# Kernel optimization log

Measured on AMD Instinct MI355X. Metric: run time of the kernel, lower is better.

The kernel has to match this reference:

```python
import jax, jax.numpy as jnp
import numpy as np

N_NODES = 50000
N_EDGES = 600000
IN_CH = 300
HID = 128
N_CLASSES = 2
N_GRAPHS = 128
BN_EPS = 1e-5


def setup_inputs() -> dict:
    key = jax.random.key(0)
    ks = jax.random.split(key, 24)
    x = jax.random.normal(ks[0], (N_NODES, IN_CH), dtype=jnp.float32)
    edge_index = jax.random.randint(ks[1], (2, N_EDGES), 0, N_NODES, dtype=jnp.int64)
    batch = jnp.sort(jax.random.randint(ks[2], (N_NODES,), 0, N_GRAPHS, dtype=jnp.int64))

    def glorot(k, shape):
        fan_in, fan_out = shape
        s = jnp.sqrt(2.0 / (fan_in + fan_out)).astype(jnp.float32)
        return jax.random.normal(k, shape, dtype=jnp.float32) * s

    inp = {"x": x, "edge_index": edge_index, "batch": batch}
    # SAGEConv params: W_l (neighbor branch), W_r (root branch), bias
    dims = [(IN_CH, HID), (HID, HID), (HID, HID)]
    for i, (din, dout) in enumerate(dims, start=1):
        inp[f"W{i}l"] = glorot(ks[3 * i], (din, dout))
        inp[f"W{i}r"] = glorot(ks[3 * i + 1], (din, dout))
        inp[f"b{i}"] = jnp.zeros((dout,), dtype=jnp.float32)
        inp[f"g{i}"] = jnp.ones((dout,), dtype=jnp.float32)   # BN gamma
        inp[f"be{i}"] = jnp.zeros((dout,), dtype=jnp.float32)  # BN beta
    inp["Wc"] = glorot(ks[20], (HID, N_CLASSES))
    inp["bc"] = jnp.zeros((N_CLASSES,), dtype=jnp.float32)
    return inp


def _sage_conv(x, src, dst, Wl, Wr, b):
    # mean-aggregate neighbor features (messages flow src -> dst)
    msg_sum = jax.ops.segment_sum(x[src], dst, num_segments=N_NODES)
    deg = jax.ops.segment_sum(jnp.ones((src.shape[0],), dtype=x.dtype), dst,
                              num_segments=N_NODES)
    mean = msg_sum / jnp.maximum(deg, 1.0)[:, None]
    return mean @ Wl + x @ Wr + b


def _bn_relu(h, gamma, beta):
    mu = jnp.mean(h, axis=0)
    var = jnp.var(h, axis=0)
    h = (h - mu) * jax.lax.rsqrt(var + BN_EPS) * gamma + beta
    return jax.nn.relu(h)


def reference(x, edge_index, batch,
              W1l, W1r, b1, g1, be1,
              W2l, W2r, b2, g2, be2,
              W3l, W3r, b3, g3, be3,
              Wc, bc):
    src, dst = edge_index[0], edge_index[1]
    h = _bn_relu(_sage_conv(x, src, dst, W1l, W1r, b1), g1, be1)
    h = _bn_relu(_sage_conv(h, src, dst, W2l, W2r, b2), g2, be2)
    h = _bn_relu(_sage_conv(h, src, dst, W3l, W3r, b3), g3, be3)
    # global mean pool per graph
    pooled = jax.ops.segment_sum(h, batch, num_segments=N_GRAPHS)
    cnt = jax.ops.segment_sum(jnp.ones((h.shape[0],), dtype=h.dtype), batch,
                              num_segments=N_GRAPHS)
    hg = pooled / jnp.maximum(cnt, 1.0)[:, None]
    out = hg @ Wc + bc
    return out, hg
```

## Files before the change

kernel.cpp:

```cpp
#include <hip/hip_runtime.h>

#define N_NODES   50000
#define N_EDGES   600000
#define IN_CH     300
#define HID       128
#define N_CLASSES 2
#define N_GRAPHS  128
#define BN_EPS    1e-5f

#define NB ((N_NODES + 511) / 512)
#define KP1 320
#define NREP 32
#define DEGB ((N_EDGES + 255) / 256)

typedef __attribute__((ext_vector_type(8))) short bf8_t;
typedef __attribute__((ext_vector_type(4))) float f4_t;

__device__ __forceinline__ unsigned short f2bf(float x) {
    union { float f; unsigned u; } q; q.f = x;
    unsigned r = q.u + 0x7fffu + ((q.u >> 16) & 1u);
    return (unsigned short)(r >> 16);
}
__device__ __forceinline__ float bf2f(unsigned short h) {
    union { float f; unsigned u; } q; q.u = ((unsigned)h) << 16; return q.f;
}

__device__ __forceinline__ void async_cp16(const void* g, void* l) {
    __builtin_amdgcn_global_load_lds(
        (const __attribute__((address_space(1))) unsigned int*)g,
        (__attribute__((address_space(3))) unsigned int*)l, 16, 0, 0);
}

__global__ __launch_bounds__(256) void deg_prepw(const int* __restrict__ dst,
                                                 int* __restrict__ ideg,
                                                 const float* __restrict__ W1l,
                                                 const float* __restrict__ W1r,
                                                 const float* __restrict__ W2l,
                                                 const float* __restrict__ W2r,
                                                 const float* __restrict__ W3l,
                                                 const float* __restrict__ W3r,
                                                 unsigned short* __restrict__ B1h,
                                                 unsigned short* __restrict__ B1l,
                                                 unsigned short* __restrict__ B2h,
                                                 unsigned short* __restrict__ B2l,
                                                 unsigned short* __restrict__ B3h,
                                                 unsigned short* __restrict__ B3l) {
    int b = blockIdx.x;
    if (b < DEGB) {
        int e = b * 256 + threadIdx.x;
        if (e < N_EDGES) atomicAdd(&ideg[dst[e]], 1);
        return;
    }
    int pb = b - DEGB;
    int layer, base;
    if (pb < 320)      { layer = 0; base = pb; }
    else if (pb < 448) { layer = 1; base = pb - 320; }
    else               { layer = 2; base = pb - 448; }
    int Kp = (layer == 0) ? KP1 : HID;
    int K  = (layer == 0) ? IN_CH : HID;
    const float* Wl = (layer == 0) ? W1l : ((layer == 1) ? W2l : W3l);
    const float* Wr = (layer == 0) ? W1r : ((layer == 1) ? W2r : W3r);
    unsigned short* Bh = (layer == 0) ? B1h : ((layer == 1) ? B2h : B3h);
    unsigned short* Bl = (layer == 0) ? B1l : ((layer == 1) ? B2l : B3l);
    int idx = base * 256 + threadIdx.x;
    int n = idx / Kp;
    int k = idx - n * Kp;
    float v = 0.f;
    if (k < K) v = (n < 128) ? Wl[k * 128 + n] : Wr[k * 128 + (n - 128)];
    unsigned short h = f2bf(v);
    unsigned short l = f2bf(v - bf2f(h));
    Bh[idx] = h;
    Bl[idx] = l;
}

__global__ __launch_bounds__(256) void scan_fused(const int* __restrict__ ideg,
                                                  int* __restrict__ row_start,
                                                  float* __restrict__ invdeg,
                                                  int* __restrict__ bsum,
                                                  int* __restrict__ bflag) {
    int b = blockIdx.x, t = threadIdx.x;
    int lane = t & 63, wv = t >> 6;
    int i0 = b * 512 + t * 2;
    int v0 = 0, v1 = 0;
    if (i0 < N_NODES) {
        int2 v = *(const int2*)&ideg[i0];
        v0 = v.x; v1 = v.y;
    }
    int tot = v0 + v1;
    int s = tot;
#pragma unroll
    for (int d = 1; d < 64; d <<= 1) {
        int u = __shfl_up(s, d);
        if (lane >= d) s += u;
    }
    __shared__ int ws[4];
    if (lane == 63) ws[wv] = s;
    __syncthreads();
    int btot = ws[0] + ws[1] + ws[2] + ws[3];
    if (t == 0) {
        atomicExch(&bsum[b], btot);
        __threadfence();
        atomicExch(&bflag[b], 1);
    }
    int part = 0;
    if (t < b) {
        while (atomicAdd(&bflag[t], 0) == 0) {}
        part = atomicAdd(&bsum[t], 0);
    }
#pragma unroll
    for (int d = 1; d < 64; d <<= 1) part += __shfl_down(part, d);
    __shared__ int ps[4];
    if (lane == 0) ps[wv] = part;
    __syncthreads();
    int boff = ps[0] + ps[1] + ps[2] + ps[3];
    int woff = 0;
    for (int w = 0; w < wv; ++w) woff += ws[w];
    int base = boff + woff + (s - tot);
    if (i0 < N_NODES) {
        row_start[i0]     = base;
        row_start[i0 + 1] = base + v0;
        invdeg[i0]     = 1.0f / fmaxf((float)v0, 1.0f);
        invdeg[i0 + 1] = 1.0f / fmaxf((float)v1, 1.0f);
    }
    if (t == 0 && b == NB - 1) row_start[N_NODES] = boff + btot;
}

__global__ __launch_bounds__(256) void fill_kernel(const int* __restrict__ src,
                                                   const int* __restrict__ dst,
                                                   const int* __restrict__ row_start,
                                                   int* __restrict__ cursor,
                                                   int* __restrict__ csr_src) {
    int e = blockIdx.x * 256 + threadIdx.x;
    if (e >= N_EDGES) return;
    int d = dst[e];
    int pos = row_start[d] + atomicAdd(&cursor[d], 1);
    csr_src[pos] = src[e];
}

__global__ __launch_bounds__(256) void gemm_mfma_x(const float* __restrict__ X,
                                                   int M,
                                                   const unsigned short* __restrict__ Bhi,
                                                   const unsigned short* __restrict__ Blo,
                                                   const float* __restrict__ bias,
                                                   unsigned short* __restrict__ C0,
                                                   float* __restrict__ C1) {
    __shared__ __align__(16) unsigned short sAh[64 * 32];
    __shared__ __align__(16) unsigned short sAl[64 * 32];
    __shared__ __align__(16) unsigned short sBh[256 * 32];
    __shared__ __align__(16) unsigned short sBl[256 * 32];

    const int tid  = threadIdx.x;
    const int lane = tid & 63;
    const int wave = tid >> 6;
    const int l16  = lane & 15;
    const int quad = lane >> 4;
    const long m0  = (long)blockIdx.x * 64;
    const int  n0  = wave * 64;

    f4_t acc[4][4];
#pragma unroll
    for (int mt = 0; mt < 4; ++mt)
#pragma unroll
        for (int nt = 0; nt < 4; ++nt) acc[mt][nt] = (f4_t){0.f, 0.f, 0.f, 0.f};

    const int ar  = tid >> 2;
    const int cl  = tid & 3;
    const int cpa = cl ^ ((ar >> 1) & 3);
    long agr = m0 + ar;
    if (agr >= M) agr = M - 1;
    const float* gX = X + agr * IN_CH;

    const int cg = ((lane & 3) ^ ((lane >> 3) & 3)) * 8;
    const unsigned short* gBh[4];
    const unsigned short* gBl[4];
    unsigned short* lBh[4];
    unsigned short* lBl[4];
#pragma unroll
    for (int j = 0; j < 4; ++j) {
        long br = wave * 64 + j * 16 + (lane >> 2);
        gBh[j] = Bhi + br * KP1 + cg;
        gBl[j] = Blo + br * KP1 + cg;
        lBh[j] = &sBh[wave * 2048 + j * 512];
        lBl[j] = &sBl[wave * 2048 + j * 512];
    }
    const int rsw = (quad ^ ((l16 >> 1) & 3)) * 8;

    for (int k0 = 0; k0 < KP1; k0 += 32) {
#pragma unroll
        for (int j = 0; j < 4; ++j) {
            async_cp16(gBh[j] + k0, lBh[j]);
            async_cp16(gBl[j] + k0, lBl[j]);
        }
        float f[8];
        const int gk = k0 + cl * 8;
#pragma unroll
        for (int hh = 0; hh < 2; ++hh) {
            int g4 = gk + hh * 4;
            float4 v = (g4 + 4 <= IN_CH) ? *(const float4*)(gX + g4)
                                         : make_float4(0.f, 0.f, 0.f, 0.f);
            f[hh * 4 + 0] = v.x; f[hh * 4 + 1] = v.y;
            f[hh * 4 + 2] = v.z; f[hh * 4 + 3] = v.w;
        }
        bf8_t h8, l8;
#pragma unroll
        for (int j = 0; j < 8; ++j) {
            unsigned short h = f2bf(f[j]);
            h8[j] = (short)h;
            l8[j] = (short)f2bf(f[j] - bf2f(h));
        }
        *(bf8_t*)&sAh[ar * 32 + cpa * 8] = h8;
        *(bf8_t*)&sAl[ar * 32 + cpa * 8] = l8;
        __syncthreads();

        bf8_t ah[4], al[4];
#pragma unroll
        for (int mt = 0; mt < 4; ++mt) {
            ah[mt] = *(const bf8_t*)&sAh[(mt * 16 + l16) * 32 + rsw];
            al[mt] = *(const bf8_t*)&sAl[(mt * 16 + l16) * 32 + rsw];
        }
#pragma unroll
        for (int nt = 0; nt < 4; ++nt) {
            bf8_t bh = *(const bf8_t*)&sBh[(n0 + nt * 16 + l16) * 32 + rsw];
            bf8_t bl = *(const bf8_t*)&sBl[(n0 + nt * 16 + l16) * 32 + rsw];
#pragma unroll
            for (int mt = 0; mt < 4; ++mt) {
                acc[mt][nt] = __builtin_amdgcn_mfma_f32_16x16x32_bf16(ah[mt], bh, acc[mt][nt], 0, 0, 0);
                acc[mt][nt] = __builtin_amdgcn_mfma_f32_16x16x32_bf16(al[mt], bh, acc[mt][nt], 0, 0, 0);
                acc[mt][nt] = __builtin_amdgcn_mfma_f32_16x16x32_bf16(ah[mt], bl, acc[mt][nt], 0, 0, 0);
            }
        }
        __syncthreads();
    }

    const bool left = (n0 < 128);
    if (left) {
        int ncol[4];
#pragma unroll
        for (int nt = 0; nt < 4; ++nt) ncol[nt] = n0 + nt * 16 + l16;
#pragma unroll
        for (int mt = 0; mt < 4; ++mt)
#pragma unroll
            for (int r = 0; r < 4; ++r) {
                long row = m0 + mt * 16 + quad * 4 + r;
                if (row < M) {
#pragma unroll
                    for (int nt = 0; nt < 4; ++nt)
                        C0[row * 128 + ncol[nt]] = f2bf(acc[mt][nt][r]);
                }
            }
    } else {
        float badd[4];
        int   ncol[4];
#pragma unroll
        for (int nt = 0; nt < 4; ++nt) {
            int ng = n0 + nt * 16 + l16 - 128;
            ncol[nt] = ng;
            badd[nt] = bias[ng];
        }
#pragma unroll
        for (int mt = 0; mt < 4; ++mt)
#pragma unroll
            for (int r = 0; r < 4; ++r) {
                long row = m0 + mt * 16 + quad * 4 + r;
                if (row < M) {
#pragma unroll
                    for (int nt = 0; nt < 4; ++nt)
                        C1[row * 128 + ncol[nt]] = acc[mt][nt][r] + badd[nt];
                }
            }
    }
}

__global__ __launch_bounds__(256) void gemm_mfma_h(const float* __restrict__ Hpre,
                                                   int M,
                                                   const float* __restrict__ rep,
                                                   const float* __restrict__ gamma,
                                                   const float* __restrict__ beta,
                                                   const unsigned short* __restrict__ Bhi,
                                                   const unsigned short* __restrict__ Blo,
                                                   const float* __restrict__ bias,
                                                   unsigned short* __restrict__ C0,
                                                   float* __restrict__ C1) {
    __shared__ __align__(16) unsigned short sAh[64 * 32];
    __shared__ __align__(16) unsigned short sAl[64 * 32];
    __shared__ __align__(16) unsigned short sBh[256 * 32];
    __shared__ __align__(16) unsigned short sBl[256 * 32];
    __shared__ float S[256];
    __shared__ float sSC[256];

    const int tid  = threadIdx.x;
    const int lane = tid & 63;
    const int wave = tid >> 6;
    const int l16  = lane & 15;
    const int quad = lane >> 4;
    const long m0  = (long)blockIdx.x * 64;
    const int  n0  = wave * 64;

    {
        float a = 0.f;
#pragma unroll
        for (int r = 0; r < NREP; ++r) a += rep[r * 256 + tid];
        S[tid] = a;
        __syncthreads();
        if (tid < HID) {
            const float invn = 1.0f / (float)N_NODES;
            float mu  = S[tid] * invn;
            float var = S[HID + tid] * invn - mu * mu;
            float sc  = gamma[tid] * rsqrtf(var + BN_EPS);
            sSC[tid]       = sc;
            sSC[HID + tid] = beta[tid] - mu * sc;
        }
        __syncthreads();
    }

    f4_t acc[4][4];
#pragma unroll
    for (int mt = 0; mt < 4; ++mt)
#pragma unroll
        for (int nt = 0; nt < 4; ++nt) acc[mt][nt] = (f4_t){0.f, 0.f, 0.f, 0.f};

    const int ar  = tid >> 2;
    const int cl  = tid & 3;
    const int cpa = cl ^ ((ar >> 1) & 3);
    long agr = m0 + ar;
    if (agr >= M) agr = M - 1;
    const float* gH = Hpre + agr * HID;

    const int cg = ((lane & 3) ^ ((lane >> 3) & 3)) * 8;
    const unsigned short* gBh[4];
    const unsigned short* gBl[4];
    unsigned short* lBh[4];
    unsigned short* lBl[4];
#pragma unroll
    for (int j = 0; j < 4; ++j) {
        long br = wave * 64 + j * 16 + (lane >> 2);
        gBh[j] = Bhi + br * HID + cg;
        gBl[j] = Blo + br * HID + cg;
        lBh[j] = &sBh[wave * 2048 + j * 512];
        lBl[j] = &sBl[wave * 2048 + j * 512];
    }
    const int rsw = (quad ^ ((l16 >> 1) & 3)) * 8;

#pragma unroll
    for (int k0 = 0; k0 < HID; k0 += 32) {
#pragma unroll
        for (int j = 0; j < 4; ++j) {
            async_cp16(gBh[j] + k0, lBh[j]);
            async_cp16(gBl[j] + k0, lBl[j]);
        }
        const int gk = k0 + cl * 8;
        float4 v0 = *(const float4*)(gH + gk);
        float4 v1 = *(const float4*)(gH + gk + 4);
        float4 s0 = *(const float4*)&sSC[gk];
        float4 s1 = *(const float4*)&sSC[gk + 4];
        float4 t0 = *(const float4*)&sSC[HID + gk];
        float4 t1 = *(const float4*)&sSC[HID + gk + 4];
        float f[8];
        f[0] = fmaxf(v0.x * s0.x + t0.x, 0.f);
        f[1] = fmaxf(v0.y * s0.y + t0.y, 0.f);
        f[2] = fmaxf(v0.z * s0.z + t0.z, 0.f);
        f[3] = fmaxf(v0.w * s0.w + t0.w, 0.f);
        f[4] = fmaxf(v1.x * s1.x + t1.x, 0.f);
        f[5] = fmaxf(v1.y * s1.y + t1.y, 0.f);
        f[6] = fmaxf(v1.z * s1.z + t1.z, 0.f);
        f[7] = fmaxf(v1.w * s1.w + t1.w, 0.f);
        bf8_t h8, l8;
#pragma unroll
        for (int j = 0; j < 8; ++j) {
            unsigned short h = f2bf(f[j]);
            h8[j] = (short)h;
            l8[j] = (short)f2bf(f[j] - bf2f(h));
        }
        *(bf8_t*)&sAh[ar * 32 + cpa * 8] = h8;
        *(bf8_t*)&sAl[ar * 32 + cpa * 8] = l8;
        __syncthreads();

        bf8_t ah[4], al[4];
#pragma unroll
        for (int mt = 0; mt < 4; ++mt) {
            ah[mt] = *(const bf8_t*)&sAh[(mt * 16 + l16) * 32 + rsw];
            al[mt] = *(const bf8_t*)&sAl[(mt * 16 + l16) * 32 + rsw];
        }
#pragma unroll
        for (int nt = 0; nt < 4; ++nt) {
            bf8_t bh = *(const bf8_t*)&sBh[(n0 + nt * 16 + l16) * 32 + rsw];
            bf8_t bl = *(const bf8_t*)&sBl[(n0 + nt * 16 + l16) * 32 + rsw];
#pragma unroll
            for (int mt = 0; mt < 4; ++mt) {
                acc[mt][nt] = __builtin_amdgcn_mfma_f32_16x16x32_bf16(ah[mt], bh, acc[mt][nt], 0, 0, 0);
                acc[mt][nt] = __builtin_amdgcn_mfma_f32_16x16x32_bf16(al[mt], bh, acc[mt][nt], 0, 0, 0);
                acc[mt][nt] = __builtin_amdgcn_mfma_f32_16x16x32_bf16(ah[mt], bl, acc[mt][nt], 0, 0, 0);
            }
        }
        __syncthreads();
    }

    const bool left = (n0 < 128);
    if (left) {
        int ncol[4];
#pragma unroll
        for (int nt = 0; nt < 4; ++nt) ncol[nt] = n0 + nt * 16 + l16;
#pragma unroll
        for (int mt = 0; mt < 4; ++mt)
#pragma unroll
            for (int r = 0; r < 4; ++r) {
                long row = m0 + mt * 16 + quad * 4 + r;
                if (row < M) {
#pragma unroll
                    for (int nt = 0; nt < 4; ++nt)
                        C0[row * 128 + ncol[nt]] = f2bf(acc[mt][nt][r]);
                }
            }
    } else {
        float badd[4];
        int   ncol[4];
#pragma unroll
        for (int nt = 0; nt < 4; ++nt) {
            int ng = n0 + nt * 16 + l16 - 128;
            ncol[nt] = ng;
            badd[nt] = bias[ng];
        }
#pragma unroll
        for (int mt = 0; mt < 4; ++mt)
#pragma unroll
            for (int r = 0; r < 4; ++r) {
                long row = m0 + mt * 16 + quad * 4 + r;
                if (row < M) {
#pragma unroll
                    for (int nt = 0; nt < 4; ++nt)
                        C1[row * 128 + ncol[nt]] = acc[mt][nt][r] + badd[nt];
                }
            }
    }
}

__global__ __launch_bounds__(256) void gather_agg(const unsigned short* __restrict__ Pl,
                                                  const int* __restrict__ row_start,
                                                  const int* __restrict__ csr_src,
                                                  const float* __restrict__ invdeg,
                                                  float* __restrict__ out,
                                                  float* __restrict__ rep) {
    int slot = threadIdx.x >> 5;
    int lane = threadIdx.x & 31;
    int node = blockIdx.x * 8 + slot;
    int beg = row_start[node];
    int end = row_start[node + 1];
    const unsigned short* base = Pl + lane * 4;
    float sx = 0.f, sy = 0.f, sz = 0.f, sw = 0.f;
    int j = beg;
    for (; j + 8 <= end; j += 8) {
        int idx[8];
#pragma unroll
        for (int u = 0; u < 8; ++u) idx[u] = csr_src[j + u];
        ushort4 v[8];
#pragma unroll
        for (int u = 0; u < 8; ++u) v[u] = *(const ushort4*)(base + (long)idx[u] * HID);
#pragma unroll
        for (int u = 0; u < 8; ++u) {
            sx += bf2f(v[u].x); sy += bf2f(v[u].y);
            sz += bf2f(v[u].z); sw += bf2f(v[u].w);
        }
    }
    if (j + 4 <= end) {
        int idx[4];
#pragma unroll
        for (int u = 0; u < 4; ++u) idx[u] = csr_src[j + u];
        ushort4 v[4];
#pragma unroll
        for (int u = 0; u < 4; ++u) v[u] = *(const ushort4*)(base + (long)idx[u] * HID);
#pragma unroll
        for (int u = 0; u < 4; ++u) {
            sx += bf2f(v[u].x); sy += bf2f(v[u].y);
            sz += bf2f(v[u].z); sw += bf2f(v[u].w);
        }
        j += 4;
    }
    for (; j < end; ++j) {
        int i0 = csr_src[j];
        ushort4 v0 = *(const ushort4*)(base + (long)i0 * HID);
        sx += bf2f(v0.x); sy += bf2f(v0.y); sz += bf2f(v0.z); sw += bf2f(v0.w);
    }
    float w = invdeg[node];
    float* o = out + (long)node * HID + lane * 4;
    float4 cur = *(float4*)o;
    cur.x += sx * w;
    cur.y += sy * w;
    cur.z += sz * w;
    cur.w += sw * w;
    *(float4*)o = cur;

    __shared__ float red[8][HID];
    float* repb = rep + (blockIdx.x & (NREP - 1)) * 256;
    *(float4*)&red[slot][lane * 4] = make_float4(cur.x, cur.y, cur.z, cur.w);
    __syncthreads();
    if (threadIdx.x < HID) {
        float tsum = 0.f;
#pragma unroll
        for (int s = 0; s < 8; ++s) tsum += red[s][threadIdx.x];
        atomicAdd(&repb[threadIdx.x], tsum);
    }
    __syncthreads();
    *(float4*)&red[slot][lane * 4] = make_float4(cur.x * cur.x, cur.y * cur.y,
                                                 cur.z * cur.z, cur.w * cur.w);
    __syncthreads();
    if (threadIdx.x < HID) {
        float tsum = 0.f;
#pragma unroll
        for (int s = 0; s < 8; ++s) tsum += red[s][threadIdx.x];
        atomicAdd(&repb[HID + threadIdx.x], tsum);
    }
}

__global__ __launch_bounds__(1024) void poolhead_bn(const float* __restrict__ h,
                                                    const int* __restrict__ batch,
                                                    const float* __restrict__ rep,
                                                    const float* __restrict__ gamma,
                                                    const float* __restrict__ beta,
                                                    const float* __restrict__ Wc,
                                                    const float* __restrict__ bc,
                                                    float* __restrict__ out) {
    __shared__ float S[256];
    __shared__ float SC[256];
    int g = blockIdx.x;
    int t = threadIdx.x;
    int c = t & 127;
    int half = t >> 7;
    if (t < 256) {
        float a = 0.f;
#pragma unroll
        for (int r = 0; r < NREP; ++r) a += rep[r * 256 + t];
        S[t] = a;
    }
    __shared__ int lo_sh, hi_sh;
    if (t == 0) {
        int lo = 0, hi = N_NODES;
        while (lo < hi) { int m = (lo + hi) >> 1; if (batch[m] < g) lo = m + 1; else hi = m; }
        lo_sh = lo;
        int lo2 = lo, hi2 = N_NODES;
        while (lo2 < hi2) { int m = (lo2 + hi2) >> 1; if (batch[m] < g + 1) lo2 = m + 1; else hi2 = m; }
        hi_sh = lo2;
    }
    __syncthreads();
    if (t < HID) {
        const float invn = 1.0f / (float)N_NODES;
        float mu  = S[t] * invn;
        float var = S[HID + t] * invn - mu * mu;
        float sc  = gamma[t] * rsqrtf(var + BN_EPS);
        SC[t]       = sc;
        SC[HID + t] = beta[t] - mu * sc;
    }
    __syncthreads();
    float bsc = SC[c], bsh = SC[HID + c];
    int lo = lo_sh, hi = hi_sh;
    float a0 = 0.f, a1 = 0.f, a2 = 0.f, a3 = 0.f;
    int r = lo + half;
    for (; r + 24 < hi; r += 32) {
        a0 += fmaxf(h[(long)(r +  0) * HID + c] * bsc + bsh, 0.f);
        a1 += fmaxf(h[(long)(r +  8) * HID + c] * bsc + bsh, 0.f);
        a2 += fmaxf(h[(long)(r + 16) * HID + c] * bsc + bsh, 0.f);
        a3 += fmaxf(h[(long)(r + 24) * HID + c] * bsc + bsh, 0.f);
    }
    for (; r < hi; r += 8) a0 += fmaxf(h[(long)r * HID + c] * bsc + bsh, 0.f);
    __shared__ float red[8][HID];
    red[half][c] = (a0 + a1) + (a2 + a3);
    __syncthreads();
    __shared__ float r0[HID], r1[HID];
    if (t < HID) {
        float inv = 1.0f / fmaxf((float)(hi - lo), 1.0f);
        float v = 0.f;
#pragma unroll
        for (int s = 0; s < 8; ++s) v += red[s][t];
        v *= inv;
        out[N_GRAPHS * N_CLASSES + g * HID + t] = v;
        r0[t] = v * Wc[t * 2 + 0];
        r1[t] = v * Wc[t * 2 + 1];
    }
    __syncthreads();
    if (t < 2) {
        const float* rr = t ? r1 : r0;
        float sum = bc[t];
        for (int i = 0; i < HID; ++i) sum += rr[i];
        out[g * 2 + t] = sum;
    }
}

extern "C" void kernel_launch(void* const* d_in, const int* in_sizes, int n_in,
                              void* d_out, int out_size, void* d_ws, size_t ws_size,
                              hipStream_t stream) {
    const float* x     = (const float*)d_in[0];
    const int*   ei    = (const int*)d_in[1];
    const int*   batch = (const int*)d_in[2];
    const float* W1l = (const float*)d_in[3];
    const float* W1r = (const float*)d_in[4];
    const float* b1  = (const float*)d_in[5];
    const float* g1  = (const float*)d_in[6];
    const float* be1 = (const float*)d_in[7];
    const float* W2l = (const float*)d_in[8];
    const float* W2r = (const float*)d_in[9];
    const float* b2  = (const float*)d_in[10];
    const float* g2  = (const float*)d_in[11];
    const float* be2 = (const float*)d_in[12];
    const float* W3l = (const float*)d_in[13];
    const float* W3r = (const float*)d_in[14];
    const float* b3  = (const float*)d_in[15];
    const float* g3  = (const float*)d_in[16];
    const float* be3 = (const float*)d_in[17];
    const float* Wc  = (const float*)d_in[18];
    const float* bc  = (const float*)d_in[19];

    const int* src = ei;
    const int* dst = ei + N_EDGES;

    float* ws = (float*)d_ws;
    const long FEAT = (long)N_NODES * HID;
    unsigned short* Pl16 = (unsigned short*)ws;
    float* buf1 = ws + FEAT;
    float* buf2 = ws + 2 * FEAT;
    int*   ideg      = (int*)(ws + 3 * FEAT);
    int*   cursor    = ideg + N_NODES;
    int*   bsum      = cursor + N_NODES;
    int*   bflag     = bsum + 128;
    int*   row_start = bflag + 128;
    int*   csr_src   = row_start + N_NODES + 4;
    float* invdeg    = (float*)(csr_src + N_EDGES);
    float* reps      = invdeg + N_NODES;
    unsigned short* B1h = (unsigned short*)(reps + 3 * NREP * 256);
    unsigned short* B1l = B1h + 256 * KP1;
    unsigned short* B2h = B1l + 256 * KP1;
    unsigned short* B2l = B2h + 256 * HID;
    unsigned short* B3h = B2l + 256 * HID;
    unsigned short* B3l = B3h + 256 * HID;

    float* outp = (float*)d_out;

    const int gemm_grid   = (N_NODES + 63) / 64;
    const int gather_grid = N_NODES / 8;
    const int dp_grid     = DEGB + 320 + 128 + 128;

    hipMemsetAsync(ideg, 0, (2 * N_NODES + 256) * sizeof(int), stream);
    hipMemsetAsync(reps, 0, 3 * NREP * 256 * sizeof(float), stream);

    deg_prepw<<<dp_grid, 256, 0, stream>>>(dst, ideg, W1l, W1r, W2l, W2r, W3l, W3r,
                                           B1h, B1l, B2h, B2l, B3h, B3l);
    scan_fused<<<NB, 256, 0, stream>>>(ideg, row_start, invdeg, bsum, bflag);
    fill_kernel<<<(N_EDGES + 255) / 256, 256, 0, stream>>>(src, dst, row_start, cursor, csr_src);

    gemm_mfma_x<<<gemm_grid, 256, 0, stream>>>(x, N_NODES, B1h, B1l, b1, Pl16, buf1);
    gather_agg<<<gather_grid, 256, 0, stream>>>(Pl16, row_start, csr_src, invdeg, buf1, reps);

    gemm_mfma_h<<<gemm_grid, 256, 0, stream>>>(buf1, N_NODES, reps, g1, be1,
                                               B2h, B2l, b2, Pl16, buf2);
    gather_agg<<<gather_grid, 256, 0, stream>>>(Pl16, row_start, csr_src, invdeg, buf2, reps + NREP * 256);

    gemm_mfma_h<<<gemm_grid, 256, 0, stream>>>(buf2, N_NODES, reps + NREP * 256, g2, be2,
                                               B3h, B3l, b3, Pl16, buf1);
    gather_agg<<<gather_grid, 256, 0, stream>>>(Pl16, row_start, csr_src, invdeg, buf1, reps + 2 * NREP * 256);

    poolhead_bn<<<N_GRAPHS, 1024, 0, stream>>>(buf1, batch, reps + 2 * NREP * 256,
                                               g3, be3, Wc, bc, outp);
}
```

Measured before the change: 399.1 us.

## Double-buffer shared-memory tiles in both MFMA GEMM kernels to overlap loads

Both GEMM kernels now prefetch the next K-tile while computing on the current one. The X-input kernel double-buffers A and B, and the H-input kernel double-buffers B with a single A buffer guarded by an extra barrier. This hides global-load latency behind the MFMA work. The cost is roughly doubled LDS usage (about 80KB per block), which may cut occupancy, and the H kernel gains an extra barrier per iteration.

```diff
diff --git a/kernel.cpp b/kernel.cpp
--- a/kernel.cpp
+++ b/kernel.cpp
@@ -144,10 +144,10 @@
                                                    const float* __restrict__ bias,
                                                    unsigned short* __restrict__ C0,
                                                    float* __restrict__ C1) {
-    __shared__ __align__(16) unsigned short sAh[64 * 32];
-    __shared__ __align__(16) unsigned short sAl[64 * 32];
-    __shared__ __align__(16) unsigned short sBh[256 * 32];
-    __shared__ __align__(16) unsigned short sBl[256 * 32];
+    __shared__ __align__(16) unsigned short sAh[2][64 * 32];
+    __shared__ __align__(16) unsigned short sAl[2][64 * 32];
+    __shared__ __align__(16) unsigned short sBh[2][256 * 32];
+    __shared__ __align__(16) unsigned short sBl[2][256 * 32];
 
     const int tid  = threadIdx.x;
     const int lane = tid & 63;
@@ -173,34 +173,34 @@
     const int cg = ((lane & 3) ^ ((lane >> 3) & 3)) * 8;
     const unsigned short* gBh[4];
     const unsigned short* gBl[4];
-    unsigned short* lBh[4];
-    unsigned short* lBl[4];
+    int lBo[4];
 #pragma unroll
     for (int j = 0; j < 4; ++j) {
         long br = wave * 64 + j * 16 + (lane >> 2);
         gBh[j] = Bhi + br * KP1 + cg;
         gBl[j] = Blo + br * KP1 + cg;
-        lBh[j] = &sBh[wave * 2048 + j * 512];
-        lBl[j] = &sBl[wave * 2048 + j * 512];
+        lBo[j] = wave * 2048 + j * 512;
     }
     const int rsw = (quad ^ ((l16 >> 1) & 3)) * 8;
 
-    for (int k0 = 0; k0 < KP1; k0 += 32) {
+    auto copyB = [&](int k0, int buf) {
 #pragma unroll
         for (int j = 0; j < 4; ++j) {
-            async_cp16(gBh[j] + k0, lBh[j]);
-            async_cp16(gBl[j] + k0, lBl[j]);
-        }
+            async_cp16(gBh[j] + k0, &sBh[buf][lBo[j]]);
+            async_cp16(gBl[j] + k0, &sBl[buf][lBo[j]]);
+        }
+    };
+    auto loadA = [&](int k0, float4& a0, float4& a1) {
+        int gk = k0 + cl * 8;
+        a0 = (gk + 4 <= IN_CH) ? *(const float4*)(gX + gk)
+                               : make_float4(0.f, 0.f, 0.f, 0.f);
+        a1 = (gk + 8 <= IN_CH) ? *(const float4*)(gX + gk + 4)
+                               : make_float4(0.f, 0.f, 0.f, 0.f);
+    };
+    auto storeA = [&](int buf, float4 a0, float4 a1) {
         float f[8];
-        const int gk = k0 + cl * 8;
-#pragma unroll
-        for (int hh = 0; hh < 2; ++hh) {
-            int g4 = gk + hh * 4;
-            float4 v = (g4 + 4 <= IN_CH) ? *(const float4*)(gX + g4)
-                                         : make_float4(0.f, 0.f, 0.f, 0.f);
-            f[hh * 4 + 0] = v.x; f[hh * 4 + 1] = v.y;
-            f[hh * 4 + 2] = v.z; f[hh * 4 + 3] = v.w;
-        }
+        f[0] = a0.x; f[1] = a0.y; f[2] = a0.z; f[3] = a0.w;
+        f[4] = a1.x; f[5] = a1.y; f[6] = a1.z; f[7] = a1.w;
         bf8_t h8, l8;
 #pragma unroll
         for (int j = 0; j < 8; ++j) {
@@ -208,20 +208,39 @@
             h8[j] = (short)h;
             l8[j] = (short)f2bf(f[j] - bf2f(h));
         }
-        *(bf8_t*)&sAh[ar * 32 + cpa * 8] = h8;
-        *(bf8_t*)&sAl[ar * 32 + cpa * 8] = l8;
-        __syncthreads();
+        *(bf8_t*)&sAh[buf][ar * 32 + cpa * 8] = h8;
+        *(bf8_t*)&sAl[buf][ar * 32 + cpa * 8] = l8;
+    };
+
+    {
+        float4 a0, a1;
+        loadA(0, a0, a1);
+        copyB(0, 0);
+        storeA(0, a0, a1);
+    }
+    __syncthreads();
+
+    const int NT = KP1 / 32;
+    int cur = 0;
+    for (int t = 0; t < NT; ++t) {
+        float4 na0 = make_float4(0.f, 0.f, 0.f, 0.f);
+        float4 na1 = make_float4(0.f, 0.f, 0.f, 0.f);
+        const bool more = (t + 1 < NT);
+        if (more) {
+            loadA((t + 1) * 32, na0, na1);
+            copyB((t + 1) * 32, cur ^ 1);
+        }
 
         bf8_t ah[4], al[4];
 #pragma unroll
         for (int mt = 0; mt < 4; ++mt) {
-            ah[mt] = *(const bf8_t*)&sAh[(mt * 16 + l16) * 32 + rsw];
-            al[mt] = *(const bf8_t*)&sAl[(mt * 16 + l16) * 32 + rsw];
+            ah[mt] = *(const bf8_t*)&sAh[cur][(mt * 16 + l16) * 32 + rsw];
+            al[mt] = *(const bf8_t*)&sAl[cur][(mt * 16 + l16) * 32 + rsw];
         }
 #pragma unroll
         for (int nt = 0; nt < 4; ++nt) {
-            bf8_t bh = *(const bf8_t*)&sBh[(n0 + nt * 16 + l16) * 32 + rsw];
-            bf8_t bl = *(const bf8_t*)&sBl[(n0 + nt * 16 + l16) * 32 + rsw];
+            bf8_t bh = *(const bf8_t*)&sBh[cur][(n0 + nt * 16 + l16) * 32 + rsw];
+            bf8_t bl = *(const bf8_t*)&sBl[cur][(n0 + nt * 16 + l16) * 32 + rsw];
 #pragma unroll
             for (int mt = 0; mt < 4; ++mt) {
                 acc[mt][nt] = __builtin_amdgcn_mfma_f32_16x16x32_bf16(ah[mt], bh, acc[mt][nt], 0, 0, 0);
@@ -229,7 +248,10 @@
                 acc[mt][nt] = __builtin_amdgcn_mfma_f32_16x16x32_bf16(ah[mt], bl, acc[mt][nt], 0, 0, 0);
             }
         }
+
+        if (more) storeA(cur ^ 1, na0, na1);
         __syncthreads();
+        cur ^= 1;
     }
 
     const bool left = (n0 < 128);
@@ -283,9 +305,8 @@
                                                    float* __restrict__ C1) {
     __shared__ __align__(16) unsigned short sAh[64 * 32];
     __shared__ __align__(16) unsigned short sAl[64 * 32];
-    __shared__ __align__(16) unsigned short sBh[256 * 32];
-    __shared__ __align__(16) unsigned short sBl[256 * 32];
-    __shared__ float S[256];
+    __shared__ __align__(16) unsigned short sBh[2][256 * 32];
+    __shared__ __align__(16) unsigned short sBl[2][256 * 32];
     __shared__ float sSC[256];
 
     const int tid  = threadIdx.x;
@@ -297,6 +318,7 @@
     const int  n0  = wave * 64;
 
     {
+        float* S = (float*)sAh;
         float a = 0.f;
 #pragma unroll
         for (int r = 0; r < NREP; ++r) a += rep[r * 256 + tid];
@@ -329,28 +351,30 @@
     const int cg = ((lane & 3) ^ ((lane >> 3) & 3)) * 8;
     const unsigned short* gBh[4];
     const unsigned short* gBl[4];
-    unsigned short* lBh[4];
-    unsigned short* lBl[4];
+    int lBo[4];
 #pragma unroll
     for (int j = 0; j < 4; ++j) {
         long br = wave * 64 + j * 16 + (lane >> 2);
         gBh[j] = Bhi + br * HID + cg;
         gBl[j] = Blo + br * HID + cg;
-        lBh[j] = &sBh[wave * 2048 + j * 512];
-        lBl[j] = &sBl[wave * 2048 + j * 512];
+        lBo[j] = wave * 2048 + j * 512;
     }
     const int rsw = (quad ^ ((l16 >> 1) & 3)) * 8;
 
-#pragma unroll
-    for (int k0 = 0; k0 < HID; k0 += 32) {
+    auto copyB = [&](int k0, int buf) {
 #pragma unroll
         for (int j = 0; j < 4; ++j) {
-            async_cp16(gBh[j] + k0, lBh[j]);
-            async_cp16(gBl[j] + k0, lBl[j]);
-        }
+            async_cp16(gBh[j] + k0, &sBh[buf][lBo[j]]);
+            async_cp16(gBl[j] + k0, &sBl[buf][lBo[j]]);
+        }
+    };
+    auto loadA = [&](int k0, float4& a0, float4& a1) {
+        int gk = k0 + cl * 8;
+        a0 = *(const float4*)(gH + gk);
+        a1 = *(const float4*)(gH + gk + 4);
+    };
+    auto storeA = [&](int k0, float4 v0, float4 v1) {
         const int gk = k0 + cl * 8;
-        float4 v0 = *(const float4*)(gH + gk);
-        float4 v1 = *(const float4*)(gH + gk + 4);
         float4 s0 = *(const float4*)&sSC[gk];
         float4 s1 = *(const float4*)&sSC[gk + 4];
         float4 t0 = *(const float4*)&sSC[HID + gk];
@@ -373,7 +397,26 @@
         }
         *(bf8_t*)&sAh[ar * 32 + cpa * 8] = h8;
         *(bf8_t*)&sAl[ar * 32 + cpa * 8] = l8;
-        __syncthreads();
+    };
+
+    {
+        float4 a0, a1;
+        loadA(0, a0, a1);
+        copyB(0, 0);
+        storeA(0, a0, a1);
+    }
+    __syncthreads();
+
+    int cur = 0;
+#pragma unroll
+    for (int t = 0; t < 4; ++t) {
+        float4 na0 = make_float4(0.f, 0.f, 0.f, 0.f);
+        float4 na1 = make_float4(0.f, 0.f, 0.f, 0.f);
+        const bool more = (t < 3);
+        if (more) {
+            loadA((t + 1) * 32, na0, na1);
+            copyB((t + 1) * 32, cur ^ 1);
+        }
 
         bf8_t ah[4], al[4];
 #pragma unroll
@@ -383,8 +426,8 @@
         }
 #pragma unroll
         for (int nt = 0; nt < 4; ++nt) {
-            bf8_t bh = *(const bf8_t*)&sBh[(n0 + nt * 16 + l16) * 32 + rsw];
-            bf8_t bl = *(const bf8_t*)&sBl[(n0 + nt * 16 + l16) * 32 + rsw];
+            bf8_t bh = *(const bf8_t*)&sBh[cur][(n0 + nt * 16 + l16) * 32 + rsw];
+            bf8_t bl = *(const bf8_t*)&sBl[cur][(n0 + nt * 16 + l16) * 32 + rsw];
 #pragma unroll
             for (int mt = 0; mt < 4; ++mt) {
                 acc[mt][nt] = __builtin_amdgcn_mfma_f32_16x16x32_bf16(ah[mt], bh, acc[mt][nt], 0, 0, 0);
@@ -392,7 +435,11 @@
                 acc[mt][nt] = __builtin_amdgcn_mfma_f32_16x16x32_bf16(ah[mt], bl, acc[mt][nt], 0, 0, 0);
             }
         }
+
         __syncthreads();
+        if (more) storeA((t + 1) * 32, na0, na1);
+        __syncthreads();
+        cur ^= 1;
     }
 
     const bool left = (n0 < 128);
```

Result: no change. 404.1 us (+1.2%).
